# Kernel optimization log

Measured on AMD Instinct MI355X. Metric: run time of the kernel, lower is better.

Reference implementation:

```python
import jax, jax.numpy as jnp
import numpy as np
import math

B, N, D, H, BS = 1, 2048, 1024, 16, 256  # batch, seq, d_model, heads, block_size


def setup_inputs() -> dict:
    key = jax.random.key(0)
    ks = jax.random.split(key, 8)
    s = 0.02  # init scale for projection weights
    return {
        "x": jax.random.normal(ks[0], (B, N, D), jnp.float32),
        "distance_bias": jax.random.uniform(ks[1], (N, N), dtype=jnp.float32),
        "Wq": jax.random.normal(ks[2], (D, D), jnp.float32) * s,
        "bq": jnp.zeros((D,), jnp.float32),
        "Wk": jax.random.normal(ks[3], (D, D), jnp.float32) * s,
        "bk": jnp.zeros((D,), jnp.float32),
        "Wv": jax.random.normal(ks[4], (D, D), jnp.float32) * s,
        "bv": jnp.zeros((D,), jnp.float32),
        "Wo": jax.random.normal(ks[5], (D, D), jnp.float32) * s,
        "bo": jnp.zeros((D,), jnp.float32),
    }


def reference(x, distance_bias, Wq, bq, Wk, bk, Wv, bv, Wo, bo):
    Bm, Nm, Dm = x.shape
    dk = Dm // H
    scale = 1.0 / math.sqrt(dk)
    nb = Nm // BS  # number of blocks along sequence

    def proj(W, b):
        # torch Linear: x @ W.T + b, then split heads -> [B, H, N, dk]
        return (x @ W.T + b).reshape(Bm, Nm, H, dk).transpose(0, 2, 1, 3)

    Q, K, V = proj(Wq, bq), proj(Wk, bk), proj(Wv, bv)

    # scores with toroidal bias subtracted (matches `scores - bias_block`)
    scores = jnp.einsum('bhqd,bhkd->bhqk', Q, K) * scale - distance_bias[None, None]
    # view as [B, H, n_qblk, BS, n_kblk, BS] and softmax PER (q-block, k-block)
    s6 = scores.reshape(Bm, H, nb, BS, nb, BS)
    w = jax.nn.softmax(s6, axis=-1)  # softmax over keys within each kv block

    Vb = V.reshape(Bm, H, nb, BS, dk)
    # sum over all kv blocks of (per-block softmax) @ V_block
    num = jnp.einsum('bhqsnk,bhnkd->bhqsd', w, Vb)  # [B,H,nb,BS,dk]
    # accumulated normalizer = sum of per-block softmax weights over all kv blocks
    norm = jnp.sum(w, axis=(4, 5))  # [B,H,nb,BS]
    O = num / (norm[..., None] + 1e-8)

    O = O.reshape(Bm, H, Nm, dk).transpose(0, 2, 1, 3).reshape(Bm, Nm, Dm)
    return O @ Wo.T + bo
```

## Files before the change

kernel.cpp:

```cpp
#include <hip/hip_runtime.h>
#include <hip/hip_fp16.h>

typedef _Float16 half8 __attribute__((ext_vector_type(8)));
typedef _Float16 half4v __attribute__((ext_vector_type(4)));
typedef float f32x4 __attribute__((ext_vector_type(4)));

#define NSEQ 2048
#define DMOD 1024
#define NHEAD 16
#define DK 64

#define GLOAD_LDS16(gp, lp) __builtin_amdgcn_global_load_lds(                 \
    (const __attribute__((address_space(1))) void*)(gp),                      \
    (__attribute__((address_space(3))) void*)(lp), 16, 0, 0)

#define WAIT_VM(n) (0xF70 | (n))


__global__ __launch_bounds__(256) void cast_pack(
    const float* __restrict__ x, const float* __restrict__ wq,
    const float* __restrict__ wk, const float* __restrict__ wv,
    const float* __restrict__ wo, _Float16* __restrict__ dst)
{
    const int w = blockIdx.x * 4 + (threadIdx.x >> 6);
    const int ln = threadIdx.x & 63, m = ln & 15, qd = ln >> 4;
    const float* src; _Float16* d; int loc;
    if (w < 4096) { src = x; d = dst; loc = w; }
    else {
        const int w2 = w - 4096, mat = w2 >> 11;
        loc = w2 & 2047;
        src = mat == 0 ? wq : mat == 1 ? wk : mat == 2 ? wv : wo;
        d = dst + 2097152 + mat * 1048576;
    }
    const int st = loc >> 5, kc = loc & 31;
    const float* p = src + (size_t)(st * 16 + m) * 1024 + kc * 32 + qd * 8;
    float4 a = *(const float4*)p, b = *(const float4*)(p + 4);
    half8 h;
    h[0] = (_Float16)a.x; h[1] = (_Float16)a.y; h[2] = (_Float16)a.z; h[3] = (_Float16)a.w;
    h[4] = (_Float16)b.x; h[5] = (_Float16)b.y; h[6] = (_Float16)b.z; h[7] = (_Float16)b.w;
    *(half8*)(d + (size_t)(loc * 64 + ln) * 8) = h;
}

__global__ __launch_bounds__(256) void cvt_bias(
    const float* __restrict__ src, _Float16* __restrict__ dst)
{
    int i = (blockIdx.x * 256 + threadIdx.x) * 4;
    float4 v = *(const float4*)(src + i);
    half4v h;
    h[0] = (_Float16)v.x; h[1] = (_Float16)v.y;
    h[2] = (_Float16)v.z; h[3] = (_Float16)v.w;
    *(half4v*)(dst + i) = h;
}

template<int BM, int BN, int MODE, bool APK>
__global__ __launch_bounds__(256) void tgemm(
    const _Float16* __restrict__ A,
    const _Float16* __restrict__ W0, const _Float16* __restrict__ W1,
    const _Float16* __restrict__ W2,
    const float* __restrict__ b0, const float* __restrict__ b1,
    const float* __restrict__ b2,
    _Float16* __restrict__ oQ, _Float16* __restrict__ oK,
    _Float16* __restrict__ oV, float* __restrict__ oF)
{
    constexpr int MT = BM / 32, NT = BN / 32;
    constexpr int NA = BM / 64, NB = BN / 64;
    __shared__ _Float16 sA[3 * BM * 32];
    __shared__ _Float16 sB[3 * BN * 32];
    const int tid = threadIdx.x, wv = tid >> 6, ln = tid & 63;
    const int m = ln & 15, qd = ln >> 4;
    const int row0 = blockIdx.x * BM;

    int sel = 0, colbase;
    const _Float16* W; const float* bias;
    if constexpr (MODE == 0) {
        sel = blockIdx.y >> 3;
        colbase = (blockIdx.y & 7) * BN;
        W = sel == 0 ? W0 : sel == 1 ? W1 : W2;
        bias = sel == 0 ? b0 : sel == 1 ? b1 : b2;
    } else {
        colbase = blockIdx.y * BN;
        W = W0; bias = b0;
    }
    const int wr = wv >> 1, wc = wv & 1;

    f32x4 acc[MT][NT];
#pragma unroll
    for (int i = 0; i < MT; ++i)
#pragma unroll
        for (int j = 0; j < NT; ++j) acc[i][j] = (f32x4){0.f, 0.f, 0.f, 0.f};

    auto stage = [&](int kc, int b) {
        _Float16* dA = sA + b * (BM * 32);
        _Float16* dB = sB + b * (BN * 32);
#pragma unroll
        for (int ra = 0; ra < NA; ++ra) {
            const int st = ra * 4 + wv;
            if constexpr (APK)
                GLOAD_LDS16(A + ((size_t)((row0 >> 4) + st) * 32 + kc) * 512 + ln * 8,
                            dA + st * 512);
            else
                GLOAD_LDS16(A + (size_t)(row0 + st * 16 + m) * 1024 + kc * 32 + qd * 8,
                            dA + st * 512);
        }
#pragma unroll
        for (int rb = 0; rb < NB; ++rb) {
            const int st = rb * 4 + wv;
            GLOAD_LDS16(W + ((size_t)((colbase >> 4) + st) * 32 + kc) * 512 + ln * 8,
                        dB + st * 512);
        }
    };
    auto step = [&](int b) {
        const _Float16* cA = sA + b * (BM * 32);
        const _Float16* cB = sB + b * (BN * 32);
        half8 af[MT], bf[NT];
#pragma unroll
        for (int i = 0; i < MT; ++i)
            af[i] = *(const half8*)(cA + ((wr * MT + i) * 64 + ln) * 8);
#pragma unroll
        for (int j = 0; j < NT; ++j)
            bf[j] = *(const half8*)(cB + ((wc * NT + j) * 64 + ln) * 8);
#pragma unroll
        for (int i = 0; i < MT; ++i)
#pragma unroll
            for (int j = 0; j < NT; ++j)
                acc[i][j] = __builtin_amdgcn_mfma_f32_16x16x32_f16(af[i], bf[j], acc[i][j], 0, 0, 0);
    };

    stage(0, 0);
    stage(1, 1);
#pragma unroll
    for (int kc = 0; kc < 31; ++kc) {
        __builtin_amdgcn_s_waitcnt(WAIT_VM(NA + NB));
        __builtin_amdgcn_s_barrier();
        if (kc < 30) stage(kc + 2, (kc + 2) % 3);
        step(kc % 3);
    }
    __builtin_amdgcn_s_waitcnt(WAIT_VM(0));
    __builtin_amdgcn_s_barrier();
    step(1);

#pragma unroll
    for (int j = 0; j < NT; ++j) {
        const int col = colbase + wc * (BN / 2) + j * 16 + m;
        const float bv = bias[col];
#pragma unroll
        for (int i = 0; i < MT; ++i) {
            const int crow0 = row0 + wr * (BM / 2) + i * 16 + qd * 4;
            if constexpr (MODE == 1) {
#pragma unroll
                for (int r = 0; r < 4; ++r)
                    oF[(size_t)(crow0 + r) * DMOD + col] = acc[i][j][r] + bv;
            } else {
                const int h = col >> 6, d = col & 63;
                if (sel == 0) {
#pragma unroll
                    for (int r = 0; r < 4; ++r)
                        oQ[h * (NSEQ * DK) + (crow0 + r) * DK + d] =
                            (_Float16)((acc[i][j][r] + bv) * 0.125f);
                } else if (sel == 1) {
#pragma unroll
                    for (int r = 0; r < 4; ++r) {
                        const int n = crow0 + r;
                        oK[(size_t)(((h * 16 + (n >> 7)) * 16
                                     + ((n >> 4) & 7) * 2 + (d >> 5)) * 64
                                    + (n & 15) + 16 * ((d >> 3) & 3)) * 8
                           + (d & 7)] = (_Float16)(acc[i][j][r] + bv);
                    }
                } else {
                    half4v hv;
#pragma unroll
                    for (int r = 0; r < 4; ++r) hv[r] = (_Float16)(acc[i][j][r] + bv);
                    const int n0 = crow0;
                    *(half4v*)(oV + (size_t)(((h * 16 + (n0 >> 7)) * 16
                                              + ((n0 >> 5) & 3) * 4 + ((d >> 4) & 3)) * 64
                                             + (d & 15) + 16 * ((n0 >> 3) & 3)) * 8
                               + (n0 & 7)) = hv;
                }
            }
        }
    }
}

__global__ __launch_bounds__(256, 2) void attn(
    const _Float16* __restrict__ Q, const _Float16* __restrict__ Kt,
    const _Float16* __restrict__ Vt, const _Float16* __restrict__ bias_h,
    _Float16* __restrict__ Ob)
{
    __shared__ _Float16 sK[2][8192];
    __shared__ _Float16 sV[2][8192];
    __shared__ _Float16 sP[8192];
    const int tid = threadIdx.x, wv = tid >> 6, ln = tid & 63;
    const int m = ln & 15, qd = ln >> 4;
    const int h = blockIdx.x;
    const int q0w = blockIdx.y * 64 + wv * 16;
    const _Float16* Qh = Q + h * (NSEQ * DK);
    const _Float16* Kh = Kt + h * (NSEQ * DK);
    const _Float16* Vh = Vt + h * (NSEQ * DK);
    const _Float16* brow = bias_h + (size_t)(q0w + m) * NSEQ;

    const half8 qf0 = *(const half8*)(Qh + (q0w + m) * DK + qd * 8);
    const half8 qf1 = *(const half8*)(Qh + (q0w + m) * DK + 32 + qd * 8);

    f32x4 oacc[4], oU[4];
#pragma unroll
    for (int v = 0; v < 4; ++v) {
        oacc[v] = (f32x4){0.f, 0.f, 0.f, 0.f};
        oU[v]   = (f32x4){0.f, 0.f, 0.f, 0.f};
    }
    float bsum = 0.f;
    half4v bcur[8], bnxt[8];

#pragma unroll
    for (int j = 0; j < 4; ++j) {
        const int f = j * 4 + wv;
        GLOAD_LDS16(Kh + f * 512 + ln * 8, &sK[0][f * 512]);
        GLOAD_LDS16(Vh + f * 512 + ln * 8, &sV[0][f * 512]);
    }
#pragma unroll
    for (int t = 0; t < 8; ++t)
        bcur[t] = *(const half4v*)(brow + t * 16 + qd * 4);
    __syncthreads();

#pragma unroll 2
    for (int step = 0; step < 16; ++step) {
        if (step < 15) {
            const _Float16* kn = Kh + (step + 1) * 8192;
            const _Float16* vn = Vh + (step + 1) * 8192;
            _Float16* dK = sK[(step + 1) & 1];
            _Float16* dV = sV[(step + 1) & 1];
#pragma unroll
            for (int j = 0; j < 4; ++j) {
                const int f = j * 4 + wv;
                GLOAD_LDS16(kn + f * 512 + ln * 8, dK + f * 512);
                GLOAD_LDS16(vn + f * 512 + ln * 8, dV + f * 512);
            }
#pragma unroll
            for (int t = 0; t < 8; ++t)
                bnxt[t] = *(const half4v*)(brow + (step + 1) * 128 + t * 16 + qd * 4);
        }

        const _Float16* cK = sK[step & 1];
        const _Float16* cV = sV[step & 1];

#pragma unroll
        for (int t = 0; t < 8; ++t) {
            half8 kf0 = *(const half8*)(cK + ((t * 2 + 0) * 64 + ln) * 8);
            half8 kf1 = *(const half8*)(cK + ((t * 2 + 1) * 64 + ln) * 8);
            f32x4 s = {0.f, 0.f, 0.f, 0.f};
            s = __builtin_amdgcn_mfma_f32_16x16x32_f16(kf0, qf0, s, 0, 0, 0);
            s = __builtin_amdgcn_mfma_f32_16x16x32_f16(kf1, qf1, s, 0, 0, 0);
            float p0 = __expf(s[0] - (float)bcur[t][0]);
            float p1 = __expf(s[1] - (float)bcur[t][1]);
            float p2 = __expf(s[2] - (float)bcur[t][2]);
            float p3 = __expf(s[3] - (float)bcur[t][3]);
            bsum += (p0 + p1) + (p2 + p3);
            half4v ph;
            ph[0] = (_Float16)p0; ph[1] = (_Float16)p1;
            ph[2] = (_Float16)p2; ph[3] = (_Float16)p3;
            *(half4v*)(sP + wv * 2048 + (t >> 1) * 512
                       + (((t & 1) * 2 + (qd >> 1)) * 16 + m) * 8
                       + (qd & 1) * 4) = ph;
        }

#pragma unroll
        for (int kk = 0; kk < 4; ++kk) {
            half8 pa = *(const half8*)(sP + wv * 2048 + kk * 512 + ln * 8);
#pragma unroll
            for (int vt = 0; vt < 4; ++vt) {
                half8 vb = *(const half8*)(cV + ((kk * 4 + vt) * 64 + ln) * 8);
                oU[vt] = __builtin_amdgcn_mfma_f32_16x16x32_f16(pa, vb, oU[vt], 0, 0, 0);
            }
        }

        if (step & 1) {
            bsum += __shfl_xor(bsum, 16, 64);
            bsum += __shfl_xor(bsum, 32, 64);
            float inv = 1.0f / (8.0f * bsum);
            float iv[4];
#pragma unroll
            for (int r = 0; r < 4; ++r) iv[r] = __shfl(inv, qd * 4 + r, 64);
#pragma unroll
            for (int vt = 0; vt < 4; ++vt) {
#pragma unroll
                for (int r = 0; r < 4; ++r) oacc[vt][r] += iv[r] * oU[vt][r];
                oU[vt] = (f32x4){0.f, 0.f, 0.f, 0.f};
            }
            bsum = 0.f;
        }

        if (step < 15) {
#pragma unroll
            for (int t = 0; t < 8; ++t) bcur[t] = bnxt[t];
        }
        __syncthreads();
    }

#pragma unroll
    for (int vt = 0; vt < 4; ++vt)
#pragma unroll
        for (int r = 0; r < 4; ++r)
            Ob[(size_t)(q0w + qd * 4 + r) * DMOD + h * DK + vt * 16 + m] =
                (_Float16)oacc[vt][r];
}

extern "C" void kernel_launch(void* const* d_in, const int* in_sizes, int n_in,
                              void* d_out, int out_size, void* d_ws, size_t ws_size,
                              hipStream_t stream)
{
    const float* x  = (const float*)d_in[0];
    const float* db = (const float*)d_in[1];
    const float* Wq = (const float*)d_in[2];
    const float* bq = (const float*)d_in[3];
    const float* Wk = (const float*)d_in[4];
    const float* bk = (const float*)d_in[5];
    const float* Wv = (const float*)d_in[6];
    const float* bv = (const float*)d_in[7];
    const float* Wo = (const float*)d_in[8];
    const float* bo = (const float*)d_in[9];
    float* out = (float*)d_out;

    _Float16* ws  = (_Float16*)d_ws;
    _Float16* xh  = ws;
    _Float16* wqh = xh  + 2097152;
    _Float16* wkh = wqh + 1048576;
    _Float16* wvh = wkh + 1048576;
    _Float16* woh = wvh + 1048576;
    _Float16* Qb  = woh + 1048576;
    _Float16* Kb  = Qb  + 2097152;
    _Float16* Vtb = Kb  + 2097152;
    _Float16* Obh = Vtb + 2097152;
    _Float16* bh  = ws;

    cast_pack<<<3072, 256, 0, stream>>>(x, Wq, Wk, Wv, Wo, xh);

    tgemm<64, 128, 0, true><<<dim3(32, 24), 256, 0, stream>>>(
        xh, wqh, wkh, wvh, bq, bk, bv, Qb, Kb, Vtb, nullptr);

    cvt_bias<<<4096, 256, 0, stream>>>(db, bh);

    attn<<<dim3(NHEAD, NSEQ / 64), 256, 0, stream>>>(Qb, Kb, Vtb, bh, Obh);

    tgemm<64, 64, 1, false><<<dim3(32, 16), 256, 0, stream>>>(
        Obh, woh, nullptr, nullptr, bo, nullptr, nullptr,
        nullptr, nullptr, nullptr, out);
}
```

Baseline: 191.3 us.

## Process two query tiles per wave in attention and pack output for GEMM

Each attention wave now handles 32 query rows (two 16-row tiles) instead of 16, so every K/V fragment read from LDS feeds two sets of MFMAs, and each block covers 128 queries. The attention output is written in the packed tile layout, which lets the output projection GEMM use the packed loader, and the GEMM tile sizes change to 128x128 for QKV and 64x128 for the output projection. The cost is higher register pressure (occupancy hint lowered to 1 block per SM), twice the LDS for P, and half as many attention blocks, which may reduce latency hiding.

```diff
diff --git a/kernel.cpp b/kernel.cpp
--- a/kernel.cpp
+++ b/kernel.cpp
@@ -52,7 +52,7 @@
     *(half4v*)(dst + i) = h;
 }
 
-template<int BM, int BN, int MODE, bool APK>
+template<int BM, int BN, int MODE>
 __global__ __launch_bounds__(256) void tgemm(
     const _Float16* __restrict__ A,
     const _Float16* __restrict__ W0, const _Float16* __restrict__ W1,
@@ -95,12 +95,8 @@
 #pragma unroll
         for (int ra = 0; ra < NA; ++ra) {
             const int st = ra * 4 + wv;
-            if constexpr (APK)
-                GLOAD_LDS16(A + ((size_t)((row0 >> 4) + st) * 32 + kc) * 512 + ln * 8,
-                            dA + st * 512);
-            else
-                GLOAD_LDS16(A + (size_t)(row0 + st * 16 + m) * 1024 + kc * 32 + qd * 8,
-                            dA + st * 512);
+            GLOAD_LDS16(A + ((size_t)((row0 >> 4) + st) * 32 + kc) * 512 + ln * 8,
+                        dA + st * 512);
         }
 #pragma unroll
         for (int rb = 0; rb < NB; ++rb) {
@@ -181,34 +177,41 @@
     }
 }
 
-__global__ __launch_bounds__(256, 2) void attn(
+__global__ __launch_bounds__(256, 1) void attn(
     const _Float16* __restrict__ Q, const _Float16* __restrict__ Kt,
     const _Float16* __restrict__ Vt, const _Float16* __restrict__ bias_h,
-    _Float16* __restrict__ Ob)
+    _Float16* __restrict__ Op)
 {
     __shared__ _Float16 sK[2][8192];
     __shared__ _Float16 sV[2][8192];
-    __shared__ _Float16 sP[8192];
+    __shared__ _Float16 sP[16384];
     const int tid = threadIdx.x, wv = tid >> 6, ln = tid & 63;
     const int m = ln & 15, qd = ln >> 4;
     const int h = blockIdx.x;
-    const int q0w = blockIdx.y * 64 + wv * 16;
+    const int q0w = blockIdx.y * 128 + wv * 32;
     const _Float16* Qh = Q + h * (NSEQ * DK);
     const _Float16* Kh = Kt + h * (NSEQ * DK);
     const _Float16* Vh = Vt + h * (NSEQ * DK);
-    const _Float16* brow = bias_h + (size_t)(q0w + m) * NSEQ;
-
-    const half8 qf0 = *(const half8*)(Qh + (q0w + m) * DK + qd * 8);
-    const half8 qf1 = *(const half8*)(Qh + (q0w + m) * DK + 32 + qd * 8);
-
-    f32x4 oacc[4], oU[4];
-#pragma unroll
-    for (int v = 0; v < 4; ++v) {
-        oacc[v] = (f32x4){0.f, 0.f, 0.f, 0.f};
-        oU[v]   = (f32x4){0.f, 0.f, 0.f, 0.f};
-    }
-    float bsum = 0.f;
-    half4v bcur[8], bnxt[8];
+    const _Float16* brow0 = bias_h + (size_t)(q0w + m) * NSEQ;
+    const _Float16* brow1 = bias_h + (size_t)(q0w + 16 + m) * NSEQ;
+
+    half8 qf[2][2];
+#pragma unroll
+    for (int u = 0; u < 2; ++u) {
+        qf[u][0] = *(const half8*)(Qh + (q0w + u * 16 + m) * DK + qd * 8);
+        qf[u][1] = *(const half8*)(Qh + (q0w + u * 16 + m) * DK + 32 + qd * 8);
+    }
+
+    f32x4 oacc[2][4], oU[2][4];
+#pragma unroll
+    for (int u = 0; u < 2; ++u)
+#pragma unroll
+        for (int v = 0; v < 4; ++v) {
+            oacc[u][v] = (f32x4){0.f, 0.f, 0.f, 0.f};
+            oU[u][v]   = (f32x4){0.f, 0.f, 0.f, 0.f};
+        }
+    float bsum[2] = {0.f, 0.f};
+    half4v bcur[2][8], bnxt[2][8];
 
 #pragma unroll
     for (int j = 0; j < 4; ++j) {
@@ -217,8 +220,10 @@
         GLOAD_LDS16(Vh + f * 512 + ln * 8, &sV[0][f * 512]);
     }
 #pragma unroll
-    for (int t = 0; t < 8; ++t)
-        bcur[t] = *(const half4v*)(brow + t * 16 + qd * 4);
+    for (int t = 0; t < 8; ++t) {
+        bcur[0][t] = *(const half4v*)(brow0 + t * 16 + qd * 4);
+        bcur[1][t] = *(const half4v*)(brow1 + t * 16 + qd * 4);
+    }
     __syncthreads();
 
 #pragma unroll 2
@@ -235,8 +240,10 @@
                 GLOAD_LDS16(vn + f * 512 + ln * 8, dV + f * 512);
             }
 #pragma unroll
-            for (int t = 0; t < 8; ++t)
-                bnxt[t] = *(const half4v*)(brow + (step + 1) * 128 + t * 16 + qd * 4);
+            for (int t = 0; t < 8; ++t) {
+                bnxt[0][t] = *(const half4v*)(brow0 + (step + 1) * 128 + t * 16 + qd * 4);
+                bnxt[1][t] = *(const half4v*)(brow1 + (step + 1) * 128 + t * 16 + qd * 4);
+            }
         }
 
         const _Float16* cK = sK[step & 1];
@@ -246,61 +253,77 @@
         for (int t = 0; t < 8; ++t) {
             half8 kf0 = *(const half8*)(cK + ((t * 2 + 0) * 64 + ln) * 8);
             half8 kf1 = *(const half8*)(cK + ((t * 2 + 1) * 64 + ln) * 8);
-            f32x4 s = {0.f, 0.f, 0.f, 0.f};
-            s = __builtin_amdgcn_mfma_f32_16x16x32_f16(kf0, qf0, s, 0, 0, 0);
-            s = __builtin_amdgcn_mfma_f32_16x16x32_f16(kf1, qf1, s, 0, 0, 0);
-            float p0 = __expf(s[0] - (float)bcur[t][0]);
-            float p1 = __expf(s[1] - (float)bcur[t][1]);
-            float p2 = __expf(s[2] - (float)bcur[t][2]);
-            float p3 = __expf(s[3] - (float)bcur[t][3]);
-            bsum += (p0 + p1) + (p2 + p3);
-            half4v ph;
-            ph[0] = (_Float16)p0; ph[1] = (_Float16)p1;
-            ph[2] = (_Float16)p2; ph[3] = (_Float16)p3;
-            *(half4v*)(sP + wv * 2048 + (t >> 1) * 512
-                       + (((t & 1) * 2 + (qd >> 1)) * 16 + m) * 8
-                       + (qd & 1) * 4) = ph;
+#pragma unroll
+            for (int u = 0; u < 2; ++u) {
+                f32x4 s = {0.f, 0.f, 0.f, 0.f};
+                s = __builtin_amdgcn_mfma_f32_16x16x32_f16(kf0, qf[u][0], s, 0, 0, 0);
+                s = __builtin_amdgcn_mfma_f32_16x16x32_f16(kf1, qf[u][1], s, 0, 0, 0);
+                float p0 = __expf(s[0] - (float)bcur[u][t][0]);
+                float p1 = __expf(s[1] - (float)bcur[u][t][1]);
+                float p2 = __expf(s[2] - (float)bcur[u][t][2]);
+                float p3 = __expf(s[3] - (float)bcur[u][t][3]);
+                bsum[u] += (p0 + p1) + (p2 + p3);
+                half4v ph;
+                ph[0] = (_Float16)p0; ph[1] = (_Float16)p1;
+                ph[2] = (_Float16)p2; ph[3] = (_Float16)p3;
+                *(half4v*)(sP + wv * 4096 + u * 2048 + (t >> 1) * 512
+                           + (((t & 1) * 2 + (qd >> 1)) * 16 + m) * 8
+                           + (qd & 1) * 4) = ph;
+            }
         }
 
 #pragma unroll
         for (int kk = 0; kk < 4; ++kk) {
-            half8 pa = *(const half8*)(sP + wv * 2048 + kk * 512 + ln * 8);
+            half8 pa0 = *(const half8*)(sP + wv * 4096 + kk * 512 + ln * 8);
+            half8 pa1 = *(const half8*)(sP + wv * 4096 + 2048 + kk * 512 + ln * 8);
 #pragma unroll
             for (int vt = 0; vt < 4; ++vt) {
                 half8 vb = *(const half8*)(cV + ((kk * 4 + vt) * 64 + ln) * 8);
-                oU[vt] = __builtin_amdgcn_mfma_f32_16x16x32_f16(pa, vb, oU[vt], 0, 0, 0);
+                oU[0][vt] = __builtin_amdgcn_mfma_f32_16x16x32_f16(pa0, vb, oU[0][vt], 0, 0, 0);
+                oU[1][vt] = __builtin_amdgcn_mfma_f32_16x16x32_f16(pa1, vb, oU[1][vt], 0, 0, 0);
             }
         }
 
         if (step & 1) {
-            bsum += __shfl_xor(bsum, 16, 64);
-            bsum += __shfl_xor(bsum, 32, 64);
-            float inv = 1.0f / (8.0f * bsum);
-            float iv[4];
-#pragma unroll
-            for (int r = 0; r < 4; ++r) iv[r] = __shfl(inv, qd * 4 + r, 64);
-#pragma unroll
-            for (int vt = 0; vt < 4; ++vt) {
-#pragma unroll
-                for (int r = 0; r < 4; ++r) oacc[vt][r] += iv[r] * oU[vt][r];
-                oU[vt] = (f32x4){0.f, 0.f, 0.f, 0.f};
-            }
-            bsum = 0.f;
+#pragma unroll
+            for (int u = 0; u < 2; ++u) {
+                float s2 = bsum[u];
+                s2 += __shfl_xor(s2, 16, 64);
+                s2 += __shfl_xor(s2, 32, 64);
+                float inv = 1.0f / (8.0f * s2);
+                float iv[4];
+#pragma unroll
+                for (int r = 0; r < 4; ++r) iv[r] = __shfl(inv, qd * 4 + r, 64);
+#pragma unroll
+                for (int vt = 0; vt < 4; ++vt) {
+#pragma unroll
+                    for (int r = 0; r < 4; ++r) oacc[u][vt][r] += iv[r] * oU[u][vt][r];
+                    oU[u][vt] = (f32x4){0.f, 0.f, 0.f, 0.f};
+                }
+                bsum[u] = 0.f;
+            }
         }
 
         if (step < 15) {
 #pragma unroll
-            for (int t = 0; t < 8; ++t) bcur[t] = bnxt[t];
+            for (int t = 0; t < 8; ++t) { bcur[0][t] = bnxt[0][t]; bcur[1][t] = bnxt[1][t]; }
         }
         __syncthreads();
     }
 
 #pragma unroll
-    for (int vt = 0; vt < 4; ++vt)
-#pragma unroll
-        for (int r = 0; r < 4; ++r)
-            Ob[(size_t)(q0w + qd * 4 + r) * DMOD + h * DK + vt * 16 + m] =
-                (_Float16)oacc[vt][r];
+    for (int u = 0; u < 2; ++u) {
+        const int st = (q0w >> 4) + u;
+#pragma unroll
+        for (int vt = 0; vt < 4; ++vt) {
+            const int d = h * 64 + vt * 16 + m;
+            _Float16* base = Op + (size_t)(st * 32 + (d >> 5)) * 512
+                             + ((d >> 3) & 3) * 128 + (d & 7);
+#pragma unroll
+            for (int r = 0; r < 4; ++r)
+                base[(qd * 4 + r) * 8] = (_Float16)oacc[u][vt][r];
+        }
+    }
 }
 
 extern "C" void kernel_launch(void* const* d_in, const int* in_sizes, int n_in,
@@ -333,14 +356,14 @@
 
     cast_pack<<<3072, 256, 0, stream>>>(x, Wq, Wk, Wv, Wo, xh);
 
-    tgemm<64, 128, 0, true><<<dim3(32, 24), 256, 0, stream>>>(
+    tgemm<128, 128, 0><<<dim3(16, 24), 256, 0, stream>>>(
         xh, wqh, wkh, wvh, bq, bk, bv, Qb, Kb, Vtb, nullptr);
 
     cvt_bias<<<4096, 256, 0, stream>>>(db, bh);
 
-    attn<<<dim3(NHEAD, NSEQ / 64), 256, 0, stream>>>(Qb, Kb, Vtb, bh, Obh);
-
-    tgemm<64, 64, 1, false><<<dim3(32, 16), 256, 0, stream>>>(
+    attn<<<dim3(NHEAD, NSEQ / 128), 256, 0, stream>>>(Qb, Kb, Vtb, bh, Obh);
+
+    tgemm<64, 128, 1><<<dim3(32, 8), 256, 0, stream>>>(
         Obh, woh, nullptr, nullptr, bo, nullptr, nullptr,
         nullptr, nullptr, nullptr, out);
 }
```

Measured after the change: 206.7 us. 8.1% more time.
